# Optimization experiments

Measured on AMD Instinct MI355X. Metric: run time of the kernel, lower is better.

## Reference

```python
import jax, jax.numpy as jnp
import numpy as np

D = 768      # model dim
H = 12       # heads
L = 6        # depth
B = 4        # batch
N = 1024     # tokens
MLP = 4      # mlp mult
DH = D // H  # head dim
EPS = 1e-5


def setup_inputs() -> dict:
    key = jax.random.key(0)
    ks = jax.random.split(key, 10)
    s = 0.02
    return {
        "x": jax.random.normal(ks[0], (B, N, D), jnp.float32),
        "spatial_weights": jax.random.normal(ks[1], (B, N, N), jnp.float32) * s,
        "ln1_g": jnp.ones((L, 1, 1, D), jnp.float32),
        "ln1_b": jnp.zeros((L, 1, 1, D), jnp.float32),
        "w_qkv": jax.random.normal(ks[2], (L, D, 3 * D), jnp.float32) * s,
        "w_out": jax.random.normal(ks[3], (L, D, D), jnp.float32) * s,
        "b_out": jnp.zeros((L, D), jnp.float32),
        "ln2_g": jnp.ones((L, 1, 1, D), jnp.float32),
        "ln2_b": jnp.zeros((L, 1, 1, D), jnp.float32),
        "w1": jax.random.normal(ks[4], (L, D, MLP * D), jnp.float32) * s,
        "b1": jnp.zeros((L, MLP * D), jnp.float32),
        "w2": jax.random.normal(ks[5], (L, MLP * D, D), jnp.float32) * s,
        "b2": jnp.zeros((L, D), jnp.float32),
    }


def _layer_norm(x, g, b):
    m = jnp.mean(x, axis=-1, keepdims=True)
    v = jnp.var(x, axis=-1, keepdims=True)  # biased, matches torch unbiased=False
    return (x - m) / jnp.sqrt(v + EPS) * g + b


def _attn(xn, sw, w_qkv, w_out, b_out):
    scale = DH ** -0.5
    qkv = xn @ w_qkv                                   # [b,n,3D]
    q, k, v = jnp.split(qkv, 3, axis=-1)
    def heads(t):  # 'b n (h d) -> h b n d'
        b, n, _ = t.shape
        return jnp.transpose(t.reshape(b, n, H, DH), (2, 0, 1, 3))
    q, k, v = heads(q), heads(k), heads(v)
    dots = jnp.einsum('hbid,hbjd->hbij', q, k) * scale
    dots = dots + sw[None]                             # spatial bias broadcast over heads
    attn = jax.nn.softmax(dots, axis=-1)
    out = jnp.einsum('hbij,hbjd->hbid', attn, v)
    out = jnp.transpose(out, (1, 2, 0, 3)).reshape(xn.shape[0], xn.shape[1], D)
    return out @ w_out + b_out


def reference(x, spatial_weights, ln1_g, ln1_b, w_qkv, w_out, b_out, ln2_g, ln2_b, w1, b1, w2, b2):
    for l in range(L):
        xn = _layer_norm(x, ln1_g[l], ln1_b[l])
        x = _attn(xn, spatial_weights, w_qkv[l], w_out[l], b_out[l]) + x
        xn = _layer_norm(x, ln2_g[l], ln2_b[l])
        h = jax.nn.gelu(xn @ w1[l] + b1[l], approximate=False)
        x = h @ w2[l] + b2[l] + x
    return x
```

## Files before the change

### kernel.cpp

```cpp
#include <hip/hip_runtime.h>
#include <hip/hip_bf16.h>

typedef __attribute__((ext_vector_type(8))) short short8;
typedef __attribute__((ext_vector_type(4))) float f32x4;

#define MFMA16(a, b, c) __builtin_amdgcn_mfma_f32_16x16x32_bf16(a, b, c, 0, 0, 0)

static __device__ __forceinline__ float gelu_f(float v) {
    return 0.5f * v * (1.0f + erff(v * 0.70710678118654752f));
}

__global__ __launch_bounds__(256) void ln_kernel(
    const float* __restrict__ x, const float* __restrict__ g, const float* __restrict__ bb,
    __hip_bfloat16* __restrict__ xn) {
    int row = blockIdx.x;
    const float* xr = x + (size_t)row * 768;
    int tid = threadIdx.x;
    float v0 = xr[tid], v1 = xr[tid + 256], v2 = xr[tid + 512];
    float s = v0 + v1 + v2;
    float s2 = v0 * v0 + v1 * v1 + v2 * v2;
    for (int m = 1; m < 64; m <<= 1) { s += __shfl_xor(s, m); s2 += __shfl_xor(s2, m); }
    __shared__ float ls[4], ls2[4];
    if ((tid & 63) == 0) { ls[tid >> 6] = s; ls2[tid >> 6] = s2; }
    __syncthreads();
    s = ls[0] + ls[1] + ls[2] + ls[3];
    s2 = ls2[0] + ls2[1] + ls2[2] + ls2[3];
    float mean = s * (1.0f / 768.0f);
    float var = s2 * (1.0f / 768.0f) - mean * mean;
    float rstd = rsqrtf(var + 1e-5f);
    __hip_bfloat16* xo = xn + (size_t)row * 768;
    xo[tid]       = __float2bfloat16((v0 - mean) * rstd * g[tid]       + bb[tid]);
    xo[tid + 256] = __float2bfloat16((v1 - mean) * rstd * g[tid + 256] + bb[tid + 256]);
    xo[tid + 512] = __float2bfloat16((v2 - mean) * rstd * g[tid + 512] + bb[tid + 512]);
}

__global__ __launch_bounds__(256) void transpose_cast_kernel(
    const float* __restrict__ in, __hip_bfloat16* __restrict__ out, int K, int N) {
    __shared__ float tile[32][33];
    size_t off = (size_t)blockIdx.z * K * N;
    in += off; out += off;
    int n0 = blockIdx.x * 32, k0 = blockIdx.y * 32;
    int tx = threadIdx.x & 31, ty = threadIdx.x >> 5;
    for (int i = ty; i < 32; i += 8)
        tile[i][tx] = in[(size_t)(k0 + i) * N + n0 + tx];
    __syncthreads();
    for (int i = ty; i < 32; i += 8)
        out[(size_t)(n0 + i) * K + k0 + tx] = __float2bfloat16(tile[tx][i]);
}

__global__ __launch_bounds__(256) void cast_bf16_kernel(
    const float* __restrict__ in, __hip_bfloat16* __restrict__ out, int n4) {
    int i = blockIdx.x * 256 + threadIdx.x;
    if (i >= n4) return;
    float4 v = ((const float4*)in)[i];
    __hip_bfloat16* o = out + (size_t)i * 4;
    o[0] = __float2bfloat16(v.x); o[1] = __float2bfloat16(v.y);
    o[2] = __float2bfloat16(v.z); o[3] = __float2bfloat16(v.w);
}

template <int EPI>
__global__ __launch_bounds__(256) void gemm_bt_kernel(
    const __hip_bfloat16* __restrict__ A, const __hip_bfloat16* __restrict__ Bt,
    const float* __restrict__ bias, const float* __restrict__ resid,
    void* __restrict__ Cout, int M, int N, int K) {
    __shared__ __hip_bfloat16 As[128 * 32];
    __shared__ __hip_bfloat16 Bs[128 * 32];
    int m0 = blockIdx.y * 128, n0 = blockIdx.x * 128;
    int tid = threadIdx.x, w = tid >> 6, lane = tid & 63;
    int quad = lane >> 4, l16 = lane & 15;
    int wm = (w & 1) * 64, wn = (w >> 1) * 64;
    f32x4 acc[4][4] = {};
    for (int kt = 0; kt < K; kt += 32) {
        __syncthreads();
        for (int c = tid; c < 512; c += 256) {
            int row = c >> 2, cc = c & 3;
            __builtin_amdgcn_global_load_lds(
                (const __attribute__((address_space(1))) void*)(A + (size_t)(m0 + row) * K + kt + cc * 8),
                (__attribute__((address_space(3))) void*)(&As[c * 8]), 16, 0, 0);
        }
        for (int c = tid; c < 512; c += 256) {
            int row = c >> 2, cc = c & 3;
            __builtin_amdgcn_global_load_lds(
                (const __attribute__((address_space(1))) void*)(Bt + (size_t)(n0 + row) * K + kt + cc * 8),
                (__attribute__((address_space(3))) void*)(&Bs[c * 8]), 16, 0, 0);
        }
        __syncthreads();
        short8 af[4], bf[4];
        for (int i = 0; i < 4; i++) {
            af[i] = *(const short8*)(As + (wm + i * 16 + l16) * 32 + quad * 8);
            bf[i] = *(const short8*)(Bs + (wn + i * 16 + l16) * 32 + quad * 8);
        }
        for (int i = 0; i < 4; i++)
            for (int j = 0; j < 4; j++)
                acc[i][j] = MFMA16(af[i], bf[j], acc[i][j]);
    }
    for (int i = 0; i < 4; i++) {
        int rbase = m0 + wm + i * 16 + quad * 4;
        for (int j = 0; j < 4; j++) {
            int col = n0 + wn + j * 16 + l16;
            float bv = (EPI >= 1) ? bias[col] : 0.0f;
            for (int r = 0; r < 4; r++) {
                size_t idx = (size_t)(rbase + r) * N + col;
                float v = acc[i][j][r] + bv;
                if (EPI == 1) v = gelu_f(v);
                if (EPI == 2) {
                    ((float*)Cout)[idx] = v + resid[idx];
                } else {
                    ((__hip_bfloat16*)Cout)[idx] = __float2bfloat16(v);
                }
            }
        }
    }
}

__global__ __launch_bounds__(256) void attn_kernel(
    const __hip_bfloat16* __restrict__ qkv, const __hip_bfloat16* __restrict__ swb,
    __hip_bfloat16* __restrict__ out) {
    int qt = blockIdx.x, h = blockIdx.y, b = blockIdx.z;
    int tid = threadIdx.x, w = tid >> 6, lane = tid & 63;
    int quad = lane >> 4, l16 = lane & 15;
    __shared__ __hip_bfloat16 Ks[64 * 72];
    __shared__ __hip_bfloat16 Vt[64 * 72];
    __shared__ __hip_bfloat16 Sw[64 * 72];
    int qrow = qt * 64 + w * 16 + l16;
    const __hip_bfloat16* qbase = qkv + (size_t)(b * 1024 + qrow) * 2304 + h * 64;
    short8 qf0 = *(const short8*)(qbase + quad * 8);
    short8 qf1 = *(const short8*)(qbase + 32 + quad * 8);
    f32x4 o[4] = {};
    float mrow[4] = {-1e30f, -1e30f, -1e30f, -1e30f};
    float lrow[4] = {0.f, 0.f, 0.f, 0.f};
    const float scale = 0.125f;
    for (int kt = 0; kt < 1024; kt += 64) {
        __syncthreads();
        for (int c = tid; c < 512; c += 256) {
            int row = c >> 3, ch = c & 7;
            size_t gb = (size_t)(b * 1024 + kt + row) * 2304 + h * 64;
            float4 kv = *(const float4*)(qkv + gb + 768 + ch * 8);
            *((float4*)(Ks + row * 72 + ch * 8)) = kv;
            float4 vv = *(const float4*)(qkv + gb + 1536 + ch * 8);
            const __hip_bfloat16* pv = (const __hip_bfloat16*)&vv;
            for (int j = 0; j < 8; j++) Vt[(ch * 8 + j) * 72 + row] = pv[j];
            float4 sv = *(const float4*)(swb + (size_t)b * 1024 * 1024 + (size_t)(qt * 64 + row) * 1024 + kt + ch * 8);
            *((float4*)(Sw + row * 72 + ch * 8)) = sv;
        }
        __syncthreads();
        f32x4 s[4];
        for (int nt = 0; nt < 4; nt++) {
            short8 kf0 = *(const short8*)(Ks + (nt * 16 + l16) * 72 + quad * 8);
            short8 kf1 = *(const short8*)(Ks + (nt * 16 + l16) * 72 + 32 + quad * 8);
            f32x4 z = {0.f, 0.f, 0.f, 0.f};
            z = MFMA16(qf0, kf0, z);
            z = MFMA16(qf1, kf1, z);
            s[nt] = z;
        }
        for (int r = 0; r < 4; r++) {
            int qloc = w * 16 + quad * 4 + r;
            float vmax = -1e30f;
            for (int nt = 0; nt < 4; nt++) {
                float sv = s[nt][r] * scale + __bfloat162float(Sw[qloc * 72 + nt * 16 + l16]);
                s[nt][r] = sv;
                vmax = fmaxf(vmax, sv);
            }
            for (int mk = 1; mk < 16; mk <<= 1) vmax = fmaxf(vmax, __shfl_xor(vmax, mk));
            float mnew = fmaxf(mrow[r], vmax);
            float alpha = __expf(mrow[r] - mnew);
            float rs = 0.f;
            for (int nt = 0; nt < 4; nt++) {
                float p = __expf(s[nt][r] - mnew);
                s[nt][r] = p;
                rs += p;
            }
            for (int mk = 1; mk < 16; mk <<= 1) rs += __shfl_xor(rs, mk);
            lrow[r] = lrow[r] * alpha + rs;
            mrow[r] = mnew;
            for (int d = 0; d < 4; d++) o[d][r] *= alpha;
        }
        for (int r = 0; r < 4; r++) {
            int qloc = w * 16 + quad * 4 + r;
            for (int nt = 0; nt < 4; nt++)
                Sw[qloc * 72 + nt * 16 + l16] = __float2bfloat16(s[nt][r]);
        }
        short8 pf0 = *(const short8*)(Sw + (w * 16 + l16) * 72 + quad * 8);
        short8 pf1 = *(const short8*)(Sw + (w * 16 + l16) * 72 + 32 + quad * 8);
        for (int d = 0; d < 4; d++) {
            short8 vf0 = *(const short8*)(Vt + (d * 16 + l16) * 72 + quad * 8);
            short8 vf1 = *(const short8*)(Vt + (d * 16 + l16) * 72 + 32 + quad * 8);
            o[d] = MFMA16(pf0, vf0, o[d]);
            o[d] = MFMA16(pf1, vf1, o[d]);
        }
    }
    for (int d = 0; d < 4; d++)
        for (int r = 0; r < 4; r++) {
            int row = qt * 64 + w * 16 + quad * 4 + r;
            out[(size_t)(b * 1024 + row) * 768 + h * 64 + d * 16 + l16] =
                __float2bfloat16(o[d][r] / lrow[r]);
        }
}

extern "C" void kernel_launch(void* const* d_in, const int* in_sizes, int n_in,
                              void* d_out, int out_size, void* d_ws, size_t ws_size,
                              hipStream_t stream) {
    const float* x_in  = (const float*)d_in[0];
    const float* sw_in = (const float*)d_in[1];
    const float* ln1_g = (const float*)d_in[2];
    const float* ln1_b = (const float*)d_in[3];
    const float* w_qkv = (const float*)d_in[4];
    const float* w_out = (const float*)d_in[5];
    const float* b_out = (const float*)d_in[6];
    const float* ln2_g = (const float*)d_in[7];
    const float* ln2_b = (const float*)d_in[8];
    const float* w1    = (const float*)d_in[9];
    const float* b1    = (const float*)d_in[10];
    const float* w2    = (const float*)d_in[11];
    const float* b2    = (const float*)d_in[12];

    char* ws = (char*)d_ws;
    size_t off = 0;
    auto alloc = [&](size_t bytes) -> void* {
        void* p = ws + off;
        off += (bytes + 255) & ~(size_t)255;
        return p;
    };
    float*          x     = (float*)alloc((size_t)4096 * 768 * 4);
    __hip_bfloat16* xn    = (__hip_bfloat16*)alloc((size_t)4096 * 768 * 2);
    __hip_bfloat16* qkv   = (__hip_bfloat16*)alloc((size_t)4096 * 2304 * 2);
    __hip_bfloat16* att   = (__hip_bfloat16*)alloc((size_t)4096 * 768 * 2);
    __hip_bfloat16* hbuf  = (__hip_bfloat16*)alloc((size_t)4096 * 3072 * 2);
    __hip_bfloat16* swb   = (__hip_bfloat16*)alloc((size_t)4 * 1024 * 1024 * 2);
    __hip_bfloat16* wqkvT = (__hip_bfloat16*)alloc((size_t)6 * 2304 * 768 * 2);
    __hip_bfloat16* woutT = (__hip_bfloat16*)alloc((size_t)6 * 768 * 768 * 2);
    __hip_bfloat16* w1T   = (__hip_bfloat16*)alloc((size_t)6 * 3072 * 768 * 2);
    __hip_bfloat16* w2T   = (__hip_bfloat16*)alloc((size_t)6 * 768 * 3072 * 2);

    hipMemcpyAsync(x, x_in, (size_t)4096 * 768 * 4, hipMemcpyDeviceToDevice, stream);
    transpose_cast_kernel<<<dim3(2304 / 32, 768 / 32, 6), 256, 0, stream>>>(w_qkv, wqkvT, 768, 2304);
    transpose_cast_kernel<<<dim3(768 / 32, 768 / 32, 6), 256, 0, stream>>>(w_out, woutT, 768, 768);
    transpose_cast_kernel<<<dim3(3072 / 32, 768 / 32, 6), 256, 0, stream>>>(w1, w1T, 768, 3072);
    transpose_cast_kernel<<<dim3(768 / 32, 3072 / 32, 6), 256, 0, stream>>>(w2, w2T, 3072, 768);
    cast_bf16_kernel<<<dim3(4 * 1024 * 1024 / 4 / 256), 256, 0, stream>>>(sw_in, swb, 4 * 1024 * 1024 / 4);

    for (int l = 0; l < 6; l++) {
        ln_kernel<<<4096, 256, 0, stream>>>(x, ln1_g + l * 768, ln1_b + l * 768, xn);
        gemm_bt_kernel<0><<<dim3(2304 / 128, 4096 / 128), 256, 0, stream>>>(
            xn, wqkvT + (size_t)l * 2304 * 768, nullptr, nullptr, qkv, 4096, 2304, 768);
        attn_kernel<<<dim3(16, 12, 4), 256, 0, stream>>>(qkv, swb, att);
        gemm_bt_kernel<2><<<dim3(768 / 128, 4096 / 128), 256, 0, stream>>>(
            att, woutT + (size_t)l * 768 * 768, b_out + l * 768, x, x, 4096, 768, 768);
        ln_kernel<<<4096, 256, 0, stream>>>(x, ln2_g + l * 768, ln2_b + l * 768, xn);
        gemm_bt_kernel<1><<<dim3(3072 / 128, 4096 / 128), 256, 0, stream>>>(
            xn, w1T + (size_t)l * 3072 * 768, b1 + l * 3072, nullptr, hbuf, 4096, 3072, 768);
        gemm_bt_kernel<2><<<dim3(768 / 128, 4096 / 128), 256, 0, stream>>>(
            hbuf, w2T + (size_t)l * 768 * 3072, b2 + l * 768, x, x, 4096, 768, 3072);
    }
    hipMemcpyAsync(d_out, x, (size_t)4096 * 768 * 4, hipMemcpyDeviceToDevice, stream);
}
```

Before: 1.788 ms.

## Split-K the N=768 GEMMs and fuse partial reduction with residual and LayerNorm

The out-projection and MLP-down GEMMs, which only launch 192 blocks, are now split along K into 2 and 4 chunks. Each chunk writes bf16 partial sums into the idle qkv buffer. A new reduce_ln kernel sums the partials, adds bias and residual, updates x, and computes the next LayerNorm in the same pass, which removes the separate LN launches and the final copy. This raises occupancy on small-N GEMMs but adds partial-sum memory traffic and rounds the partials to bf16 before accumulation, which loses some precision.

```diff
diff --git a/kernel.cpp b/kernel.cpp
--- a/kernel.cpp
+++ b/kernel.cpp
@@ -34,6 +34,55 @@
     xo[tid + 512] = __float2bfloat16((v2 - mean) * rstd * g[tid + 512] + bb[tid + 512]);
 }
 
+__global__ __launch_bounds__(256) void reduce_ln_kernel(
+    const __hip_bfloat16* __restrict__ P, int SK,
+    const float* __restrict__ bias, float* __restrict__ x,
+    const float* __restrict__ g, const float* __restrict__ bb,
+    __hip_bfloat16* __restrict__ xn) {
+    const size_t MN = (size_t)4096 * 768;
+    int row = blockIdx.x, tid = threadIdx.x;
+    float v[3];
+    float s = 0.f, s2 = 0.f;
+    for (int j = 0; j < 3; j++) {
+        int c = tid + j * 256;
+        size_t idx = (size_t)row * 768 + c;
+        float val = x[idx] + bias[c];
+        for (int sk = 0; sk < SK; sk++) val += __bfloat162float(P[(size_t)sk * MN + idx]);
+        x[idx] = val;
+        v[j] = val;
+        s += val; s2 += val * val;
+    }
+    for (int m = 1; m < 64; m <<= 1) { s += __shfl_xor(s, m); s2 += __shfl_xor(s2, m); }
+    __shared__ float ls[4], ls2[4];
+    if ((tid & 63) == 0) { ls[tid >> 6] = s; ls2[tid >> 6] = s2; }
+    __syncthreads();
+    s = ls[0] + ls[1] + ls[2] + ls[3];
+    s2 = ls2[0] + ls2[1] + ls2[2] + ls2[3];
+    float mean = s * (1.0f / 768.0f);
+    float var = s2 * (1.0f / 768.0f) - mean * mean;
+    float rstd = rsqrtf(var + 1e-5f);
+    __hip_bfloat16* xo = xn + (size_t)row * 768;
+    for (int j = 0; j < 3; j++) {
+        int c = tid + j * 256;
+        xo[c] = __float2bfloat16((v[j] - mean) * rstd * g[c] + bb[c]);
+    }
+}
+
+__global__ __launch_bounds__(256) void reduce_out_kernel(
+    const __hip_bfloat16* __restrict__ P, int SK,
+    const float* __restrict__ bias, const float* __restrict__ x,
+    float* __restrict__ out) {
+    const size_t MN = (size_t)4096 * 768;
+    int row = blockIdx.x, tid = threadIdx.x;
+    for (int j = 0; j < 3; j++) {
+        int c = tid + j * 256;
+        size_t idx = (size_t)row * 768 + c;
+        float val = x[idx] + bias[c];
+        for (int sk = 0; sk < SK; sk++) val += __bfloat162float(P[(size_t)sk * MN + idx]);
+        out[idx] = val;
+    }
+}
+
 __global__ __launch_bounds__(256) void transpose_cast_kernel(
     const float* __restrict__ in, __hip_bfloat16* __restrict__ out, int K, int N) {
     __shared__ float tile[32][33];
@@ -61,16 +110,17 @@
 template <int EPI>
 __global__ __launch_bounds__(256) void gemm_bt_kernel(
     const __hip_bfloat16* __restrict__ A, const __hip_bfloat16* __restrict__ Bt,
-    const float* __restrict__ bias, const float* __restrict__ resid,
-    void* __restrict__ Cout, int M, int N, int K) {
+    const float* __restrict__ bias,
+    void* __restrict__ Cout, int M, int N, int K, int kChunk) {
     __shared__ __hip_bfloat16 As[128 * 32];
     __shared__ __hip_bfloat16 Bs[128 * 32];
     int m0 = blockIdx.y * 128, n0 = blockIdx.x * 128;
+    int kStart = blockIdx.z * kChunk;
     int tid = threadIdx.x, w = tid >> 6, lane = tid & 63;
     int quad = lane >> 4, l16 = lane & 15;
     int wm = (w & 1) * 64, wn = (w >> 1) * 64;
     f32x4 acc[4][4] = {};
-    for (int kt = 0; kt < K; kt += 32) {
+    for (int kt = kStart; kt < kStart + kChunk; kt += 32) {
         __syncthreads();
         for (int c = tid; c < 512; c += 256) {
             int row = c >> 2, cc = c & 3;
@@ -94,20 +144,18 @@
             for (int j = 0; j < 4; j++)
                 acc[i][j] = MFMA16(af[i], bf[j], acc[i][j]);
     }
+    __hip_bfloat16* Cb = (__hip_bfloat16*)Cout;
+    if (EPI == 3) Cb += (size_t)blockIdx.z * M * N;
     for (int i = 0; i < 4; i++) {
         int rbase = m0 + wm + i * 16 + quad * 4;
         for (int j = 0; j < 4; j++) {
             int col = n0 + wn + j * 16 + l16;
-            float bv = (EPI >= 1) ? bias[col] : 0.0f;
+            float bv = (EPI == 1) ? bias[col] : 0.0f;
             for (int r = 0; r < 4; r++) {
                 size_t idx = (size_t)(rbase + r) * N + col;
                 float v = acc[i][j][r] + bv;
                 if (EPI == 1) v = gelu_f(v);
-                if (EPI == 2) {
-                    ((float*)Cout)[idx] = v + resid[idx];
-                } else {
-                    ((__hip_bfloat16*)Cout)[idx] = __float2bfloat16(v);
-                }
+                Cb[idx] = __float2bfloat16(v);
             }
         }
     }
@@ -231,6 +279,7 @@
     __hip_bfloat16* woutT = (__hip_bfloat16*)alloc((size_t)6 * 768 * 768 * 2);
     __hip_bfloat16* w1T   = (__hip_bfloat16*)alloc((size_t)6 * 3072 * 768 * 2);
     __hip_bfloat16* w2T   = (__hip_bfloat16*)alloc((size_t)6 * 768 * 3072 * 2);
+    __hip_bfloat16* P = qkv;
 
     hipMemcpyAsync(x, x_in, (size_t)4096 * 768 * 4, hipMemcpyDeviceToDevice, stream);
     transpose_cast_kernel<<<dim3(2304 / 32, 768 / 32, 6), 256, 0, stream>>>(w_qkv, wqkvT, 768, 2304);
@@ -239,18 +288,24 @@
     transpose_cast_kernel<<<dim3(768 / 32, 3072 / 32, 6), 256, 0, stream>>>(w2, w2T, 3072, 768);
     cast_bf16_kernel<<<dim3(4 * 1024 * 1024 / 4 / 256), 256, 0, stream>>>(sw_in, swb, 4 * 1024 * 1024 / 4);
 
+    ln_kernel<<<4096, 256, 0, stream>>>(x, ln1_g, ln1_b, xn);
     for (int l = 0; l < 6; l++) {
-        ln_kernel<<<4096, 256, 0, stream>>>(x, ln1_g + l * 768, ln1_b + l * 768, xn);
-        gemm_bt_kernel<0><<<dim3(2304 / 128, 4096 / 128), 256, 0, stream>>>(
-            xn, wqkvT + (size_t)l * 2304 * 768, nullptr, nullptr, qkv, 4096, 2304, 768);
+        gemm_bt_kernel<0><<<dim3(2304 / 128, 4096 / 128, 1), 256, 0, stream>>>(
+            xn, wqkvT + (size_t)l * 2304 * 768, nullptr, qkv, 4096, 2304, 768, 768);
         attn_kernel<<<dim3(16, 12, 4), 256, 0, stream>>>(qkv, swb, att);
-        gemm_bt_kernel<2><<<dim3(768 / 128, 4096 / 128), 256, 0, stream>>>(
-            att, woutT + (size_t)l * 768 * 768, b_out + l * 768, x, x, 4096, 768, 768);
-        ln_kernel<<<4096, 256, 0, stream>>>(x, ln2_g + l * 768, ln2_b + l * 768, xn);
-        gemm_bt_kernel<1><<<dim3(3072 / 128, 4096 / 128), 256, 0, stream>>>(
-            xn, w1T + (size_t)l * 3072 * 768, b1 + l * 3072, nullptr, hbuf, 4096, 3072, 768);
-        gemm_bt_kernel<2><<<dim3(768 / 128, 4096 / 128), 256, 0, stream>>>(
-            hbuf, w2T + (size_t)l * 768 * 3072, b2 + l * 768, x, x, 4096, 768, 3072);
-    }
-    hipMemcpyAsync(d_out, x, (size_t)4096 * 768 * 4, hipMemcpyDeviceToDevice, stream);
-}
+        gemm_bt_kernel<3><<<dim3(768 / 128, 4096 / 128, 2), 256, 0, stream>>>(
+            att, woutT + (size_t)l * 768 * 768, nullptr, P, 4096, 768, 768, 384);
+        reduce_ln_kernel<<<4096, 256, 0, stream>>>(
+            P, 2, b_out + l * 768, x, ln2_g + l * 768, ln2_b + l * 768, xn);
+        gemm_bt_kernel<1><<<dim3(3072 / 128, 4096 / 128, 1), 256, 0, stream>>>(
+            xn, w1T + (size_t)l * 3072 * 768, b1 + l * 3072, hbuf, 4096, 3072, 768, 768);
+        gemm_bt_kernel<3><<<dim3(768 / 128, 4096 / 128, 4), 256, 0, stream>>>(
+            hbuf, w2T + (size_t)l * 768 * 3072, nullptr, P, 4096, 768, 3072, 768);
+        if (l < 5) {
+            reduce_ln_kernel<<<4096, 256, 0, stream>>>(
+                P, 4, b2 + l * 768, x, ln1_g + (l + 1) * 768, ln1_b + (l + 1) * 768, xn);
+        } else {
+            reduce_out_kernel<<<4096, 256, 0, stream>>>(P, 4, b2 + l * 768, x, (float*)d_out);
+        }
+    }
+}
```

New measurement: 1.533 ms. -14.3%, faster.
